# Optimization experiments

Measured on AMD Instinct MI355X. Metric: run time of the kernel, lower is better.

Reference implementation:

```python
import jax, jax.numpy as jnp
import numpy as np

L = 2        # n_layers
IN = 172     # in_channels
HID = 128    # hidden_channels
NH = 4       # heads
HD = HID // NH  # per-head dim = 32
TD = 100     # time_dim
V = 400000   # global node table size
N = 150000   # sampled subgraph nodes
E = 500000   # edges per layer
B = 15000    # seed batch size


def setup_inputs() -> dict:
    key = jax.random.key(0)
    ks = jax.random.split(key, 24)
    p = lambda k, shp, s=0.05: jax.random.normal(k, shp, jnp.float32) * s
    inp = {
        "x_all": jax.random.normal(ks[0], (V, IN), jnp.float32),
        "all_node_ids": jax.random.randint(ks[1], (N,), 0, V),
        "edge_src": jax.random.randint(ks[2], (L, E), 0, N),
        "edge_dst": jax.random.randint(ks[3], (L, E), 0, N),
        "dts": jax.random.uniform(ks[4], (L, E), jnp.float32, 0.0, 1e4),
        "batch_size": B,
        # TimeEncode params
        "basis_freq": jnp.asarray(1.0 / 10 ** np.linspace(0, 9, TD), jnp.float32),
        "phase": jnp.zeros((TD,), jnp.float32),
        # input projection
        "Wp": p(ks[5], (IN, HID)), "bp": jnp.zeros((HID,), jnp.float32),
        # per-layer TransformerConv params (stacked over L)
        "Wq": p(ks[6], (L, HID, HID)), "bq": jnp.zeros((L, HID), jnp.float32),
        "Wk": p(ks[7], (L, HID, HID)), "bk": jnp.zeros((L, HID), jnp.float32),
        "Wv": p(ks[8], (L, HID, HID)), "bv": jnp.zeros((L, HID), jnp.float32),
        "We": p(ks[9], (L, TD, HID)),  # lin_edge, bias=False in PyG
        "Wskip": p(ks[10], (L, HID, HID)), "bskip": jnp.zeros((L, HID), jnp.float32),
        "bn_g": jnp.ones((L, HID), jnp.float32), "bn_b": jnp.zeros((L, HID), jnp.float32),
        # classifier head
        "W1": p(ks[11], (HID, HID)), "b1": jnp.zeros((HID,), jnp.float32),
        "g1": jnp.ones((HID,), jnp.float32), "be1": jnp.zeros((HID,), jnp.float32),
        "W2": p(ks[12], (HID, HID // 2)), "b2": jnp.zeros((HID // 2,), jnp.float32),
        "g2": jnp.ones((HID // 2,), jnp.float32), "be2": jnp.zeros((HID // 2,), jnp.float32),
        "W3": p(ks[13], (HID // 2, 1)), "b3": jnp.zeros((1,), jnp.float32),
    }
    return inp


def _bn(x, g, b):
    # BatchNorm1d, training-mode batch statistics (biased variance), eps=1e-5
    m = x.mean(0)
    v = x.var(0)
    return g * (x - m) * jax.lax.rsqrt(v + 1e-5) + b


def reference(x_all, all_node_ids, edge_src, edge_dst, dts, batch_size,
              basis_freq, phase, Wp, bp, Wq, bq, Wk, bk, Wv, bv, We,
              Wskip, bskip, bn_g, bn_b, W1, b1, g1, be1, W2, b2, g2, be2, W3, b3):
    n = all_node_ids.shape[0]
    x = x_all[all_node_ids]                      # [N, IN] gather from global table
    h = jax.nn.relu(x @ Wp + bp)                 # [N, HID]
    inv_sqrt_d = 1.0 / np.sqrt(HD)
    for i in range(L):
        src, dst, dt = edge_src[i], edge_dst[i], dts[i]
        # learnable sinusoidal time encoding of edge delta-t  [E, TD]
        te = jnp.cos(dt[:, None] * basis_freq[None, :] + phase[None, :])
        q = (h @ Wq[i] + bq[i]).reshape(n, NH, HD)
        k = (h @ Wk[i] + bk[i]).reshape(n, NH, HD)
        v = (h @ Wv[i] + bv[i]).reshape(n, NH, HD)
        e = (te @ We[i]).reshape(-1, NH, HD)     # [E, NH, HD]
        kj = k[src] + e                          # key + edge proj (PyG TransformerConv)
        vj = v[src] + e                          # value + edge proj
        alpha = jnp.einsum('ehd,ehd->eh', q[dst], kj) * inv_sqrt_d  # [E, NH]
        # scatter-softmax over edges grouped by destination node
        m = jax.ops.segment_max(alpha, dst, num_segments=n)
        a = jnp.exp(alpha - m[dst])
        s = jax.ops.segment_sum(a, dst, num_segments=n) + 1e-16
        w = a / s[dst]                           # [E, NH]
        agg = jax.ops.segment_sum(w[:, :, None] * vj, dst, num_segments=n)
        out = agg.reshape(n, HID) + h @ Wskip[i] + bskip[i]  # concat heads + root skip
        h = _bn(jax.nn.relu(out), bn_g[i], bn_b[i])          # dropout = identity (eval)
    hb = h[:batch_size]
    z = jax.nn.relu(_bn(hb @ W1 + b1, g1, be1))
    z = jax.nn.relu(_bn(z @ W2 + b2, g2, be2))
    return (z @ W3 + b3)[:, 0]                   # [batch_size]
```

## Files before the change

kernel.cpp:

```cpp
#include <hip/hip_runtime.h>
#include <hip/hip_bf16.h>
#include <math.h>

#define IN_DIM 172
#define HID 128
#define TDIM 100
#define KPAD 192

typedef __attribute__((ext_vector_type(8))) short bf16x8;
typedef __attribute__((ext_vector_type(4))) float f32x4;

static __device__ __forceinline__ ushort f2b(float x) {
  unsigned u = __float_as_uint(x);
  u += 0x7FFFu + ((u >> 16) & 1u);
  return (ushort)(u >> 16);
}
static __device__ __forceinline__ float blo(unsigned w) { return __uint_as_float(w << 16); }
static __device__ __forceinline__ float bhi(unsigned w) { return __uint_as_float(w & 0xffff0000u); }

__global__ void k_prep(const float* __restrict__ Wp,
                       const float* __restrict__ Wq, const float* __restrict__ Wk,
                       const float* __restrict__ Wv, const float* __restrict__ Ws,
                       const float* __restrict__ bq, const float* __restrict__ bk,
                       const float* __restrict__ bv, const float* __restrict__ bs,
                       const float* __restrict__ We, const float* __restrict__ W1,
                       ushort* __restrict__ wpt,
                       ushort* __restrict__ wallT0, ushort* __restrict__ wallT1,
                       float* __restrict__ ball0, float* __restrict__ ball1,
                       ushort* __restrict__ wet0, ushort* __restrict__ wet1,
                       ushort* __restrict__ w1t) {
  int i = blockIdx.x * 256 + threadIdx.x;
  if (i < 128 * KPAD) {
    int c = i / KPAD, k = i - c * KPAD;
    wpt[i] = (k < IN_DIM) ? f2b(Wp[k * HID + c]) : (ushort)0;
    return;
  }
  i -= 128 * KPAD;
  if (i < 2 * 512 * 128) {
    int layer = i >> 16;
    int j = i & 65535;
    int col = j >> 7, k = j & 127;
    int m = col >> 7, c = col & 127;
    const float* W = (m == 0) ? Wq : (m == 1) ? Wk : (m == 2) ? Wv : Ws;
    W += (size_t)layer * HID * HID;
    (layer ? wallT1 : wallT0)[j] = f2b(W[k * HID + c]);
    if (k == 0) {
      const float* bb = (m == 0) ? bq : (m == 1) ? bk : (m == 2) ? bv : bs;
      (layer ? ball1 : ball0)[col] = bb[layer * HID + c];
    }
    return;
  }
  i -= 2 * 512 * 128;
  if (i < 2 * 128 * 128) {
    int layer = i >> 14;
    int j = i & 16383;
    int c = j >> 7, t = j & 127;
    (layer ? wet1 : wet0)[j] =
        (t < TDIM) ? f2b(We[((size_t)layer * TDIM + t) * HID + c]) : (ushort)0;
    return;
  }
  i -= 2 * 128 * 128;
  if (i < 128 * 128) {
    int c = i >> 7, k = i & 127;
    w1t[i] = f2b(W1[k * HID + c]);
  }
}

__global__ __launch_bounds__(256) void k_in_mfma(
    const float* __restrict__ x_all, const int* __restrict__ ids,
    const ushort* __restrict__ wpt, const float* __restrict__ bp,
    ushort* __restrict__ h, int n) {
  __shared__ __align__(16) ushort xs[64][200];
  int tid = threadIdx.x;
  long r0 = (long)blockIdx.x * 64;
  for (int i = tid; i < 64 * 28; i += 256) {
    int r = i / 28, c = IN_DIM + (i - r * 28);
    xs[r][c] = 0;
  }
  for (int i = tid; i < 64 * 43; i += 256) {
    int r = i / 43, seg = i - r * 43;
    long row = r0 + r;
    float4 v = make_float4(0.f, 0.f, 0.f, 0.f);
    if (row < n) v = *(const float4*)(x_all + (size_t)ids[row] * IN_DIM + seg * 4);
    ushort4 u;
    u.x = f2b(v.x); u.y = f2b(v.y); u.z = f2b(v.z); u.w = f2b(v.w);
    *(ushort4*)&xs[r][seg * 4] = u;
  }
  __syncthreads();
  int wv = tid >> 6, l = tid & 63;
  int arow = wv * 16 + (l & 15);
  int kb0 = (l >> 4) * 8;
  bf16x8 a[6];
  #pragma unroll
  for (int kk = 0; kk < 6; ++kk) a[kk] = *(const bf16x8*)&xs[arow][kk * 32 + kb0];
  #pragma unroll
  for (int nt = 0; nt < 8; ++nt) {
    int col = nt * 16 + (l & 15);
    const ushort* wcol = wpt + (size_t)col * KPAD + kb0;
    f32x4 acc = {0.f, 0.f, 0.f, 0.f};
    #pragma unroll
    for (int kk = 0; kk < 6; ++kk) {
      bf16x8 bfr = *(const bf16x8*)(wcol + kk * 32);
      acc = __builtin_amdgcn_mfma_f32_16x16x32_bf16(a[kk], bfr, acc, 0, 0, 0);
    }
    float bias = bp[col];
    #pragma unroll
    for (int j = 0; j < 4; ++j) {
      long row = r0 + wv * 16 + (l >> 4) * 4 + j;
      if (row < n) {
        float y = acc[j] + bias;
        h[row * HID + col] = f2b(y > 0.f ? y : 0.f);
      }
    }
  }
}

template <bool BN_IN>
__global__ __launch_bounds__(512) void k_qkvs(
    const ushort* __restrict__ hbf, const float* __restrict__ xf,
    const float* __restrict__ sums, const float* __restrict__ bng,
    const float* __restrict__ bnb, float inv_n,
    const ushort* __restrict__ wallT, const float* __restrict__ ball,
    ushort* __restrict__ qb, ushort* __restrict__ kbuf, ushort* __restrict__ vb,
    float* __restrict__ ob, int n) {
  __shared__ __align__(16) ushort hs[128][136];
  __shared__ __align__(16) ushort ws[64][136];
  __shared__ float As[128], Bs[128];
  int tid = threadIdx.x;
  if (BN_IN) {
    if (tid < 128) {
      float mean = sums[tid] * inv_n;
      float var = sums[128 + tid] * inv_n - mean * mean;
      float A = bng[tid] * rsqrtf(var + 1e-5f);
      As[tid] = A;
      Bs[tid] = bnb[tid] - mean * A;
    }
    __syncthreads();
  }
  long r0 = (long)blockIdx.x * 128;
  for (int i = tid; i < 128 * 16; i += 512) {
    int r = i >> 4, cseg = i & 15;
    long row = r0 + r;
    int c0 = cseg * 8;
    if (BN_IN) {
      ushort4 ua = {0, 0, 0, 0}, ub = {0, 0, 0, 0};
      if (row < n) {
        const float* xr = xf + row * HID + c0;
        float4 xa = *(const float4*)xr;
        float4 xb = *(const float4*)(xr + 4);
        ua.x = f2b(As[c0 + 0] * fmaxf(xa.x, 0.f) + Bs[c0 + 0]);
        ua.y = f2b(As[c0 + 1] * fmaxf(xa.y, 0.f) + Bs[c0 + 1]);
        ua.z = f2b(As[c0 + 2] * fmaxf(xa.z, 0.f) + Bs[c0 + 2]);
        ua.w = f2b(As[c0 + 3] * fmaxf(xa.w, 0.f) + Bs[c0 + 3]);
        ub.x = f2b(As[c0 + 4] * fmaxf(xb.x, 0.f) + Bs[c0 + 4]);
        ub.y = f2b(As[c0 + 5] * fmaxf(xb.y, 0.f) + Bs[c0 + 5]);
        ub.z = f2b(As[c0 + 6] * fmaxf(xb.z, 0.f) + Bs[c0 + 6]);
        ub.w = f2b(As[c0 + 7] * fmaxf(xb.w, 0.f) + Bs[c0 + 7]);
      }
      *(ushort4*)&hs[r][c0] = ua;
      *(ushort4*)&hs[r][c0 + 4] = ub;
    } else {
      bf16x8 zv = {0, 0, 0, 0, 0, 0, 0, 0};
      bf16x8 v = (row < n) ? *(const bf16x8*)&hbf[row * HID + c0] : zv;
      *(bf16x8*)&hs[r][c0] = v;
    }
  }
  __syncthreads();
  int wv = tid >> 6, l = tid & 63;
  int arow = wv * 16 + (l & 15);
  int kb0 = (l >> 4) * 8;
  bf16x8 a[4];
  #pragma unroll
  for (int kk = 0; kk < 4; ++kk) a[kk] = *(const bf16x8*)&hs[arow][kk * 32 + kb0];

  for (int g = 0; g < 8; ++g) {
    __syncthreads();
    for (int i = tid; i < 64 * 16; i += 512) {
      int c = i >> 4, cseg = i & 15;
      *(bf16x8*)&ws[c][cseg * 8] =
          *(const bf16x8*)&wallT[(size_t)(g * 64 + c) * 128 + cseg * 8];
    }
    __syncthreads();
    #pragma unroll
    for (int nt = 0; nt < 4; ++nt) {
      int colc = nt * 16 + (l & 15);
      int gcol = g * 64 + colc;
      f32x4 acc = {0.f, 0.f, 0.f, 0.f};
      #pragma unroll
      for (int kk = 0; kk < 4; ++kk) {
        bf16x8 bfr = *(const bf16x8*)&ws[colc][kk * 32 + kb0];
        acc = __builtin_amdgcn_mfma_f32_16x16x32_bf16(a[kk], bfr, acc, 0, 0, 0);
      }
      float bias = ball[gcol];
      int m = gcol >> 7, c = gcol & 127;
      #pragma unroll
      for (int j = 0; j < 4; ++j) {
        long row = r0 + wv * 16 + (l >> 4) * 4 + j;
        if (row < n) {
          float y = acc[j] + bias;
          if (m == 3) ob[row * HID + c] = y;
          else {
            ushort* db = (m == 0) ? qb : (m == 1) ? kbuf : vb;
            db[row * HID + c] = f2b(y);
          }
        }
      }
    }
  }
}

__global__ __launch_bounds__(256) void k_mfma128_bn(
    const float* __restrict__ xf, const float* __restrict__ sums,
    const float* __restrict__ bng, const float* __restrict__ bnb, float inv_n,
    const ushort* __restrict__ WT, const float* __restrict__ bias,
    float* __restrict__ Y, int n) {
  __shared__ __align__(16) ushort hs[64][136];
  __shared__ float As[128], Bs[128];
  int tid = threadIdx.x;
  if (tid < 128) {
    float mean = sums[tid] * inv_n;
    float var = sums[128 + tid] * inv_n - mean * mean;
    float A = bng[tid] * rsqrtf(var + 1e-5f);
    As[tid] = A;
    Bs[tid] = bnb[tid] - mean * A;
  }
  __syncthreads();
  long r0 = (long)blockIdx.x * 64;
  for (int i = tid; i < 64 * 16; i += 256) {
    int r = i >> 4, cseg = i & 15;
    long row = r0 + r;
    int c0 = cseg * 8;
    ushort4 ua = {0, 0, 0, 0}, ub = {0, 0, 0, 0};
    if (row < n) {
      const float* xr = xf + row * HID + c0;
      float4 xa = *(const float4*)xr;
      float4 xb = *(const float4*)(xr + 4);
      ua.x = f2b(As[c0 + 0] * fmaxf(xa.x, 0.f) + Bs[c0 + 0]);
      ua.y = f2b(As[c0 + 1] * fmaxf(xa.y, 0.f) + Bs[c0 + 1]);
      ua.z = f2b(As[c0 + 2] * fmaxf(xa.z, 0.f) + Bs[c0 + 2]);
      ua.w = f2b(As[c0 + 3] * fmaxf(xa.w, 0.f) + Bs[c0 + 3]);
      ub.x = f2b(As[c0 + 4] * fmaxf(xb.x, 0.f) + Bs[c0 + 4]);
      ub.y = f2b(As[c0 + 5] * fmaxf(xb.y, 0.f) + Bs[c0 + 5]);
      ub.z = f2b(As[c0 + 6] * fmaxf(xb.z, 0.f) + Bs[c0 + 6]);
      ub.w = f2b(As[c0 + 7] * fmaxf(xb.w, 0.f) + Bs[c0 + 7]);
    }
    *(ushort4*)&hs[r][c0] = ua;
    *(ushort4*)&hs[r][c0 + 4] = ub;
  }
  __syncthreads();
  int wv = tid >> 6, l = tid & 63;
  int arow = wv * 16 + (l & 15);
  int kb0 = (l >> 4) * 8;
  bf16x8 a[4];
  #pragma unroll
  for (int kk = 0; kk < 4; ++kk) a[kk] = *(const bf16x8*)&hs[arow][kk * 32 + kb0];
  #pragma unroll
  for (int nt = 0; nt < 8; ++nt) {
    int col = nt * 16 + (l & 15);
    const ushort* wcol = WT + (size_t)col * 128 + kb0;
    f32x4 acc = {0.f, 0.f, 0.f, 0.f};
    #pragma unroll
    for (int kk = 0; kk < 4; ++kk) {
      bf16x8 bfr = *(const bf16x8*)(wcol + kk * 32);
      acc = __builtin_amdgcn_mfma_f32_16x16x32_bf16(a[kk], bfr, acc, 0, 0, 0);
    }
    float bs = bias[col];
    #pragma unroll
    for (int j = 0; j < 4; ++j) {
      long row = r0 + wv * 16 + (l >> 4) * 4 + j;
      if (row < n) Y[row * HID + col] = acc[j] + bs;
    }
  }
}

__global__ void k_hist(const int* __restrict__ dst, int* __restrict__ counts, int nE) {
  int e = blockIdx.x * 256 + threadIdx.x;
  if (e < nE) atomicAdd(&counts[dst[e]], 1);
}

__global__ void k_scan_chunk(const int* __restrict__ counts, int* __restrict__ offs,
                             int* __restrict__ chunkSums, int n) {
  __shared__ int ls[256];
  int t = threadIdx.x;
  int base = blockIdx.x * 1024 + t * 4;
  int v[4];
  #pragma unroll
  for (int j = 0; j < 4; ++j) v[j] = (base + j < n) ? counts[base + j] : 0;
  ls[t] = v[0] + v[1] + v[2] + v[3];
  __syncthreads();
  for (int off = 1; off < 256; off <<= 1) {
    int x = (t >= off) ? ls[t - off] : 0;
    __syncthreads();
    ls[t] += x;
    __syncthreads();
  }
  int run = (t == 0) ? 0 : ls[t - 1];
  if (t == 255) chunkSums[blockIdx.x] = ls[255];
  #pragma unroll
  for (int j = 0; j < 4; ++j) {
    if (base + j < n) offs[base + j] = run;
    run += v[j];
  }
}

__global__ void k_scan_tops(int* __restrict__ chunkSums, int nchunks) {
  __shared__ int ls[256];
  int t = threadIdx.x;
  ls[t] = (t < nchunks) ? chunkSums[t] : 0;
  __syncthreads();
  for (int off = 1; off < 256; off <<= 1) {
    int x = (t >= off) ? ls[t - off] : 0;
    __syncthreads();
    ls[t] += x;
    __syncthreads();
  }
  int excl = (t == 0) ? 0 : ls[t - 1];
  if (t < nchunks) chunkSums[t] = excl;
}

__global__ void k_scan_add(int* __restrict__ offs, const int* __restrict__ chunkSums,
                           int n, int nE) {
  int i = blockIdx.x * 256 + threadIdx.x;
  if (i < n) offs[i] += chunkSums[i >> 10];
  if (i == 0) offs[n] = nE;
}

__global__ void k_scatter(const int* __restrict__ src, const int* __restrict__ dst,
                          const float* __restrict__ dts, const int* __restrict__ offs,
                          int* __restrict__ cursor, uint2* __restrict__ edata, int nE) {
  int e = blockIdx.x * 256 + threadIdx.x;
  if (e >= nE) return;
  int d = dst[e];
  int pos = offs[d] + atomicAdd(&cursor[d], 1);
  edata[pos] = make_uint2((unsigned)src[e], __float_as_uint(dts[e]));
}

__global__ __launch_bounds__(256) void k_te_mfma(
    const uint2* __restrict__ edata, const float* __restrict__ freq,
    const float* __restrict__ phase, const ushort* __restrict__ wet,
    ushort* __restrict__ eb, int nE) {
  __shared__ __align__(16) ushort te[64][136];
  __shared__ float dt_s[64];
  __shared__ float fr_s[128], ph_s[128];
  int tid = threadIdx.x;
  if (tid < 128) {
    fr_s[tid] = (tid < TDIM) ? freq[tid] : 0.f;
    ph_s[tid] = (tid < TDIM) ? phase[tid] : 0.f;
  }
  long e0 = (long)blockIdx.x << 6;
  if (tid < 64) dt_s[tid] = (e0 + tid < nE) ? __uint_as_float(edata[e0 + tid].y) : 0.f;
  __syncthreads();
  for (int i = tid; i < 64 * 128; i += 256) {
    int el = i >> 7, t = i & 127;
    float val = (t < TDIM) ? __cosf(dt_s[el] * fr_s[t] + ph_s[t]) : 0.f;
    te[el][t] = f2b(val);
  }
  __syncthreads();
  int wv = tid >> 6, l = tid & 63;
  int arow = wv * 16 + (l & 15);
  int kb0 = (l >> 4) * 8;
  bf16x8 a[4];
  #pragma unroll
  for (int kk = 0; kk < 4; ++kk) a[kk] = *(const bf16x8*)&te[arow][kk * 32 + kb0];
  #pragma unroll
  for (int nt = 0; nt < 8; ++nt) {
    int col = nt * 16 + (l & 15);
    const ushort* wcol = wet + (size_t)col * 128 + kb0;
    f32x4 acc = {0.f, 0.f, 0.f, 0.f};
    #pragma unroll
    for (int kk = 0; kk < 4; ++kk) {
      bf16x8 bfr = *(const bf16x8*)(wcol + kk * 32);
      acc = __builtin_amdgcn_mfma_f32_16x16x32_bf16(a[kk], bfr, acc, 0, 0, 0);
    }
    #pragma unroll
    for (int j = 0; j < 4; ++j) {
      long row = e0 + wv * 16 + (l >> 4) * 4 + j;
      if (row < nE) eb[row * 128 + col] = f2b(acc[j]);
    }
  }
}

__global__ void k_attn(const int* __restrict__ offs, const uint2* __restrict__ edata,
                       const ushort* __restrict__ eb, const ushort* __restrict__ qb,
                       const ushort* __restrict__ kb, const ushort* __restrict__ vb,
                       float* __restrict__ ob, int n) {
  int d = (blockIdx.x * 256 + threadIdx.x) >> 6;
  if (d >= n) return;
  int lane = threadIdx.x & 63;
  int sub = lane >> 4;
  int cl = lane & 15;
  int c0 = cl * 8;
  int beg = offs[d], end = offs[d + 1];
  if (beg == end) return;
  uint4 qw = *(const uint4*)(qb + (size_t)d * HID + c0);
  float q0 = blo(qw.x), q1 = bhi(qw.x), q2 = blo(qw.y), q3 = bhi(qw.y);
  float q4 = blo(qw.z), q5 = bhi(qw.z), q6 = blo(qw.w), q7 = bhi(qw.w);
  float m = -INFINITY, s = 0.f;
  float a0 = 0.f, a1 = 0.f, a2 = 0.f, a3 = 0.f, a4 = 0.f, a5 = 0.f, a6 = 0.f, a7 = 0.f;
  for (int base = beg; base < end; base += 4) {
    int pos = base + sub;
    bool valid = pos < end;
    int pp = valid ? pos : beg;
    int sv = (int)edata[pp].x;
    uint4 kw = *(const uint4*)(kb + (size_t)sv * HID + c0);
    uint4 vw = *(const uint4*)(vb + (size_t)sv * HID + c0);
    uint4 ew = *(const uint4*)(eb + (size_t)pp * HID + c0);
    float e0 = blo(ew.x), e1 = bhi(ew.x), e2 = blo(ew.y), e3 = bhi(ew.y);
    float e4 = blo(ew.z), e5 = bhi(ew.z), e6 = blo(ew.w), e7 = bhi(ew.w);
    float p = q0 * (blo(kw.x) + e0) + q1 * (bhi(kw.x) + e1) +
              q2 * (blo(kw.y) + e2) + q3 * (bhi(kw.y) + e3) +
              q4 * (blo(kw.z) + e4) + q5 * (bhi(kw.z) + e5) +
              q6 * (blo(kw.w) + e6) + q7 * (bhi(kw.w) + e7);
    p += __shfl_xor(p, 1);
    p += __shfl_xor(p, 2);
    float av = valid ? p * 0.17677669529663687f : -INFINITY;
    float nm = fmaxf(m, av);
    float sc = (m > -INFINITY) ? __expf(m - nm) : 0.f;
    float pe = valid ? __expf(av - nm) : 0.f;
    m = nm;
    s = s * sc + pe;
    a0 = a0 * sc + pe * (blo(vw.x) + e0);
    a1 = a1 * sc + pe * (bhi(vw.x) + e1);
    a2 = a2 * sc + pe * (blo(vw.y) + e2);
    a3 = a3 * sc + pe * (bhi(vw.y) + e3);
    a4 = a4 * sc + pe * (blo(vw.z) + e4);
    a5 = a5 * sc + pe * (bhi(vw.z) + e5);
    a6 = a6 * sc + pe * (blo(vw.w) + e6);
    a7 = a7 * sc + pe * (bhi(vw.w) + e7);
  }
  #pragma unroll
  for (int off = 16; off <= 32; off <<= 1) {
    float mo = __shfl_xor(m, off);
    float so = __shfl_xor(s, off);
    float t0 = __shfl_xor(a0, off), t1 = __shfl_xor(a1, off);
    float t2 = __shfl_xor(a2, off), t3 = __shfl_xor(a3, off);
    float t4 = __shfl_xor(a4, off), t5 = __shfl_xor(a5, off);
    float t6 = __shfl_xor(a6, off), t7 = __shfl_xor(a7, off);
    float nm = fmaxf(m, mo);
    float s1 = (m > -INFINITY) ? __expf(m - nm) : 0.f;
    float s2 = (mo > -INFINITY) ? __expf(mo - nm) : 0.f;
    s = s * s1 + so * s2;
    a0 = a0 * s1 + t0 * s2; a1 = a1 * s1 + t1 * s2;
    a2 = a2 * s1 + t2 * s2; a3 = a3 * s1 + t3 * s2;
    a4 = a4 * s1 + t4 * s2; a5 = a5 * s1 + t5 * s2;
    a6 = a6 * s1 + t6 * s2; a7 = a7 * s1 + t7 * s2;
    m = nm;
  }
  if (sub == 0) {
    float inv = 1.f / (s + 1e-16f);
    float4* o = (float4*)(ob + (size_t)d * HID + c0);
    float4 x0 = o[0], x1 = o[1];
    x0.x += a0 * inv; x0.y += a1 * inv; x0.z += a2 * inv; x0.w += a3 * inv;
    x1.x += a4 * inv; x1.y += a5 * inv; x1.z += a6 * inv; x1.w += a7 * inv;
    o[0] = x0; o[1] = x1;
  }
}

template <bool PRE_RELU>
__global__ void k_bn_reduce(const float* __restrict__ X, int n, int C, int shift,
                            float* __restrict__ sums) {
  int col = threadIdx.x & (C - 1);
  int rloc = threadIdx.x >> shift;
  int rpt = 256 >> shift;
  float s = 0.f, s2 = 0.f;
  for (long r = (long)blockIdx.x * rpt + rloc; r < n; r += (long)gridDim.x * rpt) {
    float v = X[r * C + col];
    if (PRE_RELU) v = v > 0.f ? v : 0.f;
    s += v; s2 += v * v;
  }
  __shared__ float ls[256], ls2[256];
  ls[threadIdx.x] = s; ls2[threadIdx.x] = s2;
  __syncthreads();
  if (rloc == 0) {
    for (int j = 1; j < rpt; ++j) { s += ls[j * C + col]; s2 += ls2[j * C + col]; }
    atomicAdd(&sums[col], s);
    atomicAdd(&sums[C + col], s2);
  }
}

__global__ __launch_bounds__(256) void k_gemm_64(
    const float* __restrict__ X, const float* __restrict__ sums,
    const float* __restrict__ g, const float* __restrict__ be, float inv_n,
    const float* __restrict__ W, const float* __restrict__ b,
    float* __restrict__ Y, int n) {
  __shared__ float xs[16][HID];
  __shared__ float As[128], Bs[128];
  if (threadIdx.x < 128) {
    int c = threadIdx.x;
    float mean = sums[c] * inv_n;
    float var = sums[128 + c] * inv_n - mean * mean;
    float A = g[c] * rsqrtf(var + 1e-5f);
    As[c] = A;
    Bs[c] = be[c] - mean * A;
  }
  __syncthreads();
  int r0 = blockIdx.x * 16;
  for (int idx = threadIdx.x; idx < 16 * HID; idx += 256) {
    int r = idx >> 7, c = idx & 127;
    int row = r0 + r;
    float v = (row < n) ? X[(size_t)row * HID + c] : 0.f;
    v = As[c] * v + Bs[c];
    xs[r][c] = v > 0.f ? v : 0.f;
  }
  __syncthreads();
  int col = threadIdx.x & 63;
  int rg = threadIdx.x >> 6;
  float acc[4] = {0.f, 0.f, 0.f, 0.f};
  #pragma unroll 4
  for (int kk = 0; kk < HID; ++kk) {
    float w = W[kk * 64 + col];
    #pragma unroll
    for (int j = 0; j < 4; ++j) acc[j] += xs[rg + 4 * j][kk] * w;
  }
  float bias = b[col];
  #pragma unroll
  for (int j = 0; j < 4; ++j) {
    int row = r0 + rg + 4 * j;
    if (row < n) Y[(size_t)row * 64 + col] = acc[j] + bias;
  }
}

__global__ __launch_bounds__(256) void k_final(
    const float* __restrict__ z2, const float* __restrict__ sums,
    const float* __restrict__ g2, const float* __restrict__ be2, float inv_n,
    const float* __restrict__ W3, const float* __restrict__ b3,
    float* __restrict__ out, int n) {
  int wave = threadIdx.x >> 6, lane = threadIdx.x & 63;
  int row = blockIdx.x * 4 + wave;
  if (row >= n) return;
  float z = z2[(size_t)row * 64 + lane];
  float mean = sums[lane] * inv_n;
  float var = sums[64 + lane] * inv_n - mean * mean;
  float v = g2[lane] * (z - mean) * rsqrtf(var + 1e-5f) + be2[lane];
  v = v > 0.f ? v : 0.f;
  float pv = v * W3[lane];
  pv += __shfl_xor(pv, 1);
  pv += __shfl_xor(pv, 2);
  pv += __shfl_xor(pv, 4);
  pv += __shfl_xor(pv, 8);
  pv += __shfl_xor(pv, 16);
  pv += __shfl_xor(pv, 32);
  if (lane == 0) out[row] = pv + b3[0];
}

extern "C" void kernel_launch(void* const* d_in, const int* in_sizes, int n_in,
                              void* d_out, int out_size, void* d_ws, size_t ws_size,
                              hipStream_t stream) {
  const float* x_all = (const float*)d_in[0];
  const int* ids = (const int*)d_in[1];
  const int* esrc = (const int*)d_in[2];
  const int* edst = (const int*)d_in[3];
  const float* dts = (const float*)d_in[4];
  const float* freq = (const float*)d_in[6];
  const float* phase = (const float*)d_in[7];
  const float* Wp = (const float*)d_in[8];
  const float* bp = (const float*)d_in[9];
  const float* Wq = (const float*)d_in[10];
  const float* bq = (const float*)d_in[11];
  const float* Wk = (const float*)d_in[12];
  const float* bk = (const float*)d_in[13];
  const float* Wv = (const float*)d_in[14];
  const float* bv = (const float*)d_in[15];
  const float* We = (const float*)d_in[16];
  const float* Wskip = (const float*)d_in[17];
  const float* bskip = (const float*)d_in[18];
  const float* bn_g = (const float*)d_in[19];
  const float* bn_b = (const float*)d_in[20];
  const float* W1 = (const float*)d_in[21];
  const float* b1 = (const float*)d_in[22];
  const float* g1 = (const float*)d_in[23];
  const float* be1 = (const float*)d_in[24];
  const float* W2 = (const float*)d_in[25];
  const float* b2 = (const float*)d_in[26];
  const float* g2 = (const float*)d_in[27];
  const float* be2 = (const float*)d_in[28];
  const float* W3 = (const float*)d_in[29];
  const float* b3 = (const float*)d_in[30];

  size_t n = (size_t)in_sizes[1];
  size_t nE = (size_t)in_sizes[2] / 2;
  int B = out_size;

  char* pc = (char*)d_ws;
  auto alloc = [&](size_t bytes) { char* r = pc; pc += (bytes + 255) & ~(size_t)255; return r; };
  ushort* h    = (ushort*)alloc(n * HID * 2);
  ushort* qb   = (ushort*)alloc(n * HID * 2);
  ushort* kb   = (ushort*)alloc(n * HID * 2);
  ushort* vb   = (ushort*)alloc(n * HID * 2);
  float*  ob0  = (float*)alloc(n * HID * 4);
  float*  ob1  = (float*)alloc(n * HID * 4);
  ushort* eb   = (ushort*)alloc(nE * HID * 2);
  uint2* edata = (uint2*)alloc(nE * 8);
  int* offs    = (int*)alloc((n + 1) * 4);
  int* chunkS  = (int*)alloc(256 * 4);
  size_t zbytes = 4 * n * 4 + 4 * 256 * 4;
  char* zb = alloc(zbytes);
  int* counts0 = (int*)zb;
  int* cursor0 = counts0 + n;
  int* counts1 = cursor0 + n;
  int* cursor1 = counts1 + n;
  float* sumsL0 = (float*)(cursor1 + n);
  float* sumsL1 = sumsL0 + 256;
  float* sumsZ1 = sumsL1 + 256;
  float* sumsZ2 = sumsZ1 + 256;
  ushort* wpt    = (ushort*)alloc(128 * KPAD * 2);
  ushort* wallT0 = (ushort*)alloc(512 * 128 * 2);
  ushort* wallT1 = (ushort*)alloc(512 * 128 * 2);
  float* ball0   = (float*)alloc(512 * 4);
  float* ball1   = (float*)alloc(512 * 4);
  ushort* wet0   = (ushort*)alloc(128 * 128 * 2);
  ushort* wet1   = (ushort*)alloc(128 * 128 * 2);
  ushort* w1t    = (ushort*)alloc(128 * 128 * 2);
  float* z1      = (float*)alloc((size_t)B * HID * 4);
  float* z2      = (float*)alloc((size_t)B * 64 * 4);

  int gn64 = (int)((n + 63) / 64);
  int gn128 = (int)((n + 127) / 128);
  int ge256 = (int)((nE + 255) / 256);
  int eblk = (int)((nE + 63) / 64);
  int nchunks = (int)((n + 1023) / 1024);
  float inv_nf = 1.f / (float)n;
  float inv_bf = 1.f / (float)B;

  hipMemsetAsync(zb, 0, zbytes, stream);
  k_prep<<<(128 * KPAD + 2 * 512 * 128 + 2 * 128 * 128 + 128 * 128 + 255) / 256, 256, 0, stream>>>(
      Wp, Wq, Wk, Wv, Wskip, bq, bk, bv, bskip, We, W1,
      wpt, wallT0, wallT1, ball0, ball1, wet0, wet1, w1t);
  k_in_mfma<<<gn64, 256, 0, stream>>>(x_all, ids, wpt, bp, h, (int)n);

  for (int i = 0; i < 2; ++i) {
    const int* src_i = esrc + i * nE;
    const int* dst_i = edst + i * nE;
    const float* dts_i = dts + i * nE;
    int* counts = i ? counts1 : counts0;
    int* cursor = i ? cursor1 : cursor0;
    const ushort* wallT = i ? wallT1 : wallT0;
    const float* ball = i ? ball1 : ball0;
    const ushort* wet = i ? wet1 : wet0;
    float* ob = i ? ob1 : ob0;

    if (i == 0)
      k_qkvs<false><<<gn128, 512, 0, stream>>>(h, nullptr, nullptr, nullptr, nullptr, 0.f,
                                               wallT, ball, qb, kb, vb, ob, (int)n);
    else
      k_qkvs<true><<<gn128, 512, 0, stream>>>(nullptr, ob0, sumsL0, bn_g, bn_b, inv_nf,
                                              wallT, ball, qb, kb, vb, ob, (int)n);

    k_hist<<<ge256, 256, 0, stream>>>(dst_i, counts, (int)nE);
    k_scan_chunk<<<nchunks, 256, 0, stream>>>(counts, offs, chunkS, (int)n);
    k_scan_tops<<<1, 256, 0, stream>>>(chunkS, nchunks);
    k_scan_add<<<(int)((n + 255) / 256), 256, 0, stream>>>(offs, chunkS, (int)n, (int)nE);
    k_scatter<<<ge256, 256, 0, stream>>>(src_i, dst_i, dts_i, offs, cursor, edata, (int)nE);
    k_te_mfma<<<eblk, 256, 0, stream>>>(edata, freq, phase, wet, eb, (int)nE);
    k_attn<<<(int)((n + 3) / 4), 256, 0, stream>>>(offs, edata, eb, qb, kb, vb, ob, (int)n);
    k_bn_reduce<true><<<512, 256, 0, stream>>>(ob, (int)n, HID, 7, i ? sumsL1 : sumsL0);
  }

  k_mfma128_bn<<<(B + 63) / 64, 256, 0, stream>>>(ob1, sumsL1, bn_g + HID, bn_b + HID,
                                                  inv_nf, w1t, b1, z1, B);
  k_bn_reduce<false><<<512, 256, 0, stream>>>(z1, B, HID, 7, sumsZ1);
  k_gemm_64<<<(B + 15) / 16, 256, 0, stream>>>(z1, sumsZ1, g1, be1, inv_bf, W2, b2, z2, B);
  k_bn_reduce<false><<<512, 256, 0, stream>>>(z2, B, 64, 6, sumsZ2);
  k_final<<<(B + 3) / 4, 256, 0, stream>>>(z2, sumsZ2, g2, be2, inv_bf, W3, b3,
                                           (float*)d_out, B);
}
```

Baseline: 1.023 ms.

## Interleave K/V storage, batch CSR build for both layers, register-resident QKVS weights

K and V are stored interleaved in one buffer, so each gathered source row fetches K and V from adjacent memory. The histogram, scan and scatter for both layers are merged into single launches over a combined 2n segment space, which removes the per-layer launch overhead. The QKVS GEMM now keeps each wave's 64 weight columns in registers and loops over row tiles, dropping the per-group LDS weight staging and its barriers. The cost is higher register pressure and larger CSR and edge buffers.

Result: no change. 1.030 ms (+0.7%).

```diff
diff --git a/kernel.cpp b/kernel.cpp
--- a/kernel.cpp
+++ b/kernel.cpp
@@ -121,10 +121,9 @@
     const float* __restrict__ sums, const float* __restrict__ bng,
     const float* __restrict__ bnb, float inv_n,
     const ushort* __restrict__ wallT, const float* __restrict__ ball,
-    ushort* __restrict__ qb, ushort* __restrict__ kbuf, ushort* __restrict__ vb,
+    ushort* __restrict__ qb, ushort* __restrict__ kvb,
     float* __restrict__ ob, int n) {
   __shared__ __align__(16) ushort hs[128][136];
-  __shared__ __align__(16) ushort ws[64][136];
   __shared__ float As[128], Bs[128];
   int tid = threadIdx.x;
   if (BN_IN) {
@@ -165,44 +164,48 @@
       *(bf16x8*)&hs[r][c0] = v;
     }
   }
-  __syncthreads();
   int wv = tid >> 6, l = tid & 63;
-  int arow = wv * 16 + (l & 15);
   int kb0 = (l >> 4) * 8;
-  bf16x8 a[4];
-  #pragma unroll
-  for (int kk = 0; kk < 4; ++kk) a[kk] = *(const bf16x8*)&hs[arow][kk * 32 + kb0];
-
-  for (int g = 0; g < 8; ++g) {
-    __syncthreads();
-    for (int i = tid; i < 64 * 16; i += 512) {
-      int c = i >> 4, cseg = i & 15;
-      *(bf16x8*)&ws[c][cseg * 8] =
-          *(const bf16x8*)&wallT[(size_t)(g * 64 + c) * 128 + cseg * 8];
-    }
-    __syncthreads();
-    #pragma unroll
-    for (int nt = 0; nt < 4; ++nt) {
-      int colc = nt * 16 + (l & 15);
-      int gcol = g * 64 + colc;
-      f32x4 acc = {0.f, 0.f, 0.f, 0.f};
+  int Cw = wv * 64;
+  int m = wv >> 1;
+  bf16x8 b[4][4];
+  float bias4[4];
+  #pragma unroll
+  for (int ct = 0; ct < 4; ++ct) {
+    int col = Cw + ct * 16 + (l & 15);
+    bias4[ct] = ball[col];
+    #pragma unroll
+    for (int kk = 0; kk < 4; ++kk)
+      b[ct][kk] = *(const bf16x8*)&wallT[(size_t)col * 128 + kk * 32 + kb0];
+  }
+  __syncthreads();
+  #pragma unroll 2
+  for (int rt = 0; rt < 8; ++rt) {
+    bf16x8 a[4];
+    #pragma unroll
+    for (int kk = 0; kk < 4; ++kk)
+      a[kk] = *(const bf16x8*)&hs[rt * 16 + (l & 15)][kk * 32 + kb0];
+    f32x4 acc[4];
+    #pragma unroll
+    for (int ct = 0; ct < 4; ++ct) acc[ct] = (f32x4){0.f, 0.f, 0.f, 0.f};
+    #pragma unroll
+    for (int kk = 0; kk < 4; ++kk) {
       #pragma unroll
-      for (int kk = 0; kk < 4; ++kk) {
-        bf16x8 bfr = *(const bf16x8*)&ws[colc][kk * 32 + kb0];
-        acc = __builtin_amdgcn_mfma_f32_16x16x32_bf16(a[kk], bfr, acc, 0, 0, 0);
-      }
-      float bias = ball[gcol];
-      int m = gcol >> 7, c = gcol & 127;
+      for (int ct = 0; ct < 4; ++ct)
+        acc[ct] = __builtin_amdgcn_mfma_f32_16x16x32_bf16(a[kk], b[ct][kk], acc[ct], 0, 0, 0);
+    }
+    #pragma unroll
+    for (int ct = 0; ct < 4; ++ct) {
+      int cc = (wv & 1) * 64 + ct * 16 + (l & 15);
       #pragma unroll
       for (int j = 0; j < 4; ++j) {
-        long row = r0 + wv * 16 + (l >> 4) * 4 + j;
+        long row = r0 + rt * 16 + (l >> 4) * 4 + j;
         if (row < n) {
-          float y = acc[j] + bias;
-          if (m == 3) ob[row * HID + c] = y;
-          else {
-            ushort* db = (m == 0) ? qb : (m == 1) ? kbuf : vb;
-            db[row * HID + c] = f2b(y);
-          }
+          float y = acc[ct][j] + bias4[ct];
+          if (m == 0) qb[row * HID + cc] = f2b(y);
+          else if (m == 1) kvb[row * 256 + cc] = f2b(y);
+          else if (m == 2) kvb[row * 256 + 128 + cc] = f2b(y);
+          else ob[row * HID + cc] = y;
         }
       }
     }
@@ -273,19 +276,22 @@
   }
 }
 
-__global__ void k_hist(const int* __restrict__ dst, int* __restrict__ counts, int nE) {
+__global__ void k_hist2(const int* __restrict__ dst_all, int* __restrict__ counts,
+                        int n, int nE2, int nE) {
   int e = blockIdx.x * 256 + threadIdx.x;
-  if (e < nE) atomicAdd(&counts[dst[e]], 1);
+  if (e >= nE2) return;
+  int layer = (e >= nE) ? 1 : 0;
+  atomicAdd(&counts[layer * n + dst_all[e]], 1);
 }
 
 __global__ void k_scan_chunk(const int* __restrict__ counts, int* __restrict__ offs,
-                             int* __restrict__ chunkSums, int n) {
+                             int* __restrict__ chunkSums, int m) {
   __shared__ int ls[256];
   int t = threadIdx.x;
   int base = blockIdx.x * 1024 + t * 4;
   int v[4];
   #pragma unroll
-  for (int j = 0; j < 4; ++j) v[j] = (base + j < n) ? counts[base + j] : 0;
+  for (int j = 0; j < 4; ++j) v[j] = (base + j < m) ? counts[base + j] : 0;
   ls[t] = v[0] + v[1] + v[2] + v[3];
   __syncthreads();
   for (int off = 1; off < 256; off <<= 1) {
@@ -298,17 +304,17 @@
   if (t == 255) chunkSums[blockIdx.x] = ls[255];
   #pragma unroll
   for (int j = 0; j < 4; ++j) {
-    if (base + j < n) offs[base + j] = run;
+    if (base + j < m) offs[base + j] = run;
     run += v[j];
   }
 }
 
-__global__ void k_scan_tops(int* __restrict__ chunkSums, int nchunks) {
-  __shared__ int ls[256];
+__global__ __launch_bounds__(512) void k_scan_tops(int* __restrict__ chunkSums, int nchunks) {
+  __shared__ int ls[512];
   int t = threadIdx.x;
   ls[t] = (t < nchunks) ? chunkSums[t] : 0;
   __syncthreads();
-  for (int off = 1; off < 256; off <<= 1) {
+  for (int off = 1; off < 512; off <<= 1) {
     int x = (t >= off) ? ls[t - off] : 0;
     __syncthreads();
     ls[t] += x;
@@ -319,20 +325,22 @@
 }
 
 __global__ void k_scan_add(int* __restrict__ offs, const int* __restrict__ chunkSums,
-                           int n, int nE) {
+                           int m, int totalE) {
   int i = blockIdx.x * 256 + threadIdx.x;
-  if (i < n) offs[i] += chunkSums[i >> 10];
-  if (i == 0) offs[n] = nE;
-}
-
-__global__ void k_scatter(const int* __restrict__ src, const int* __restrict__ dst,
-                          const float* __restrict__ dts, const int* __restrict__ offs,
-                          int* __restrict__ cursor, uint2* __restrict__ edata, int nE) {
+  if (i < m) offs[i] += chunkSums[i >> 10];
+  if (i == 0) offs[m] = totalE;
+}
+
+__global__ void k_scatter2(const int* __restrict__ src_all, const int* __restrict__ dst_all,
+                           const float* __restrict__ dts_all, const int* __restrict__ offs,
+                           int* __restrict__ cursor, uint2* __restrict__ edata,
+                           int n, int nE2, int nE) {
   int e = blockIdx.x * 256 + threadIdx.x;
-  if (e >= nE) return;
-  int d = dst[e];
+  if (e >= nE2) return;
+  int layer = (e >= nE) ? 1 : 0;
+  int d = layer * n + dst_all[e];
   int pos = offs[d] + atomicAdd(&cursor[d], 1);
-  edata[pos] = make_uint2((unsigned)src[e], __float_as_uint(dts[e]));
+  edata[pos] = make_uint2((unsigned)src_all[e], __float_as_uint(dts_all[e]));
 }
 
 __global__ __launch_bounds__(256) void k_te_mfma(
@@ -380,9 +388,9 @@
   }
 }
 
-__global__ void k_attn(const int* __restrict__ offs, const uint2* __restrict__ edata,
-                       const ushort* __restrict__ eb, const ushort* __restrict__ qb,
-                       const ushort* __restrict__ kb, const ushort* __restrict__ vb,
+__global__ void k_attn(const int* __restrict__ offs_l, const uint2* __restrict__ edata,
+                       int bias, const ushort* __restrict__ eb,
+                       const ushort* __restrict__ qb, const ushort* __restrict__ kvb,
                        float* __restrict__ ob, int n) {
   int d = (blockIdx.x * 256 + threadIdx.x) >> 6;
   if (d >= n) return;
@@ -390,8 +398,9 @@
   int sub = lane >> 4;
   int cl = lane & 15;
   int c0 = cl * 8;
-  int beg = offs[d], end = offs[d + 1];
+  int beg = offs_l[d], end = offs_l[d + 1];
   if (beg == end) return;
+  const ushort* ebl = eb - (size_t)bias * HID;
   uint4 qw = *(const uint4*)(qb + (size_t)d * HID + c0);
   float q0 = blo(qw.x), q1 = bhi(qw.x), q2 = blo(qw.y), q3 = bhi(qw.y);
   float q4 = blo(qw.z), q5 = bhi(qw.z), q6 = blo(qw.w), q7 = bhi(qw.w);
@@ -402,9 +411,9 @@
     bool valid = pos < end;
     int pp = valid ? pos : beg;
     int sv = (int)edata[pp].x;
-    uint4 kw = *(const uint4*)(kb + (size_t)sv * HID + c0);
-    uint4 vw = *(const uint4*)(vb + (size_t)sv * HID + c0);
-    uint4 ew = *(const uint4*)(eb + (size_t)pp * HID + c0);
+    uint4 kw = *(const uint4*)(kvb + (size_t)sv * 256 + c0);
+    uint4 vw = *(const uint4*)(kvb + (size_t)sv * 256 + 128 + c0);
+    uint4 ew = *(const uint4*)(ebl + (size_t)pp * HID + c0);
     float e0 = blo(ew.x), e1 = bhi(ew.x), e2 = blo(ew.y), e3 = bhi(ew.y);
     float e4 = blo(ew.z), e5 = bhi(ew.z), e6 = blo(ew.w), e7 = bhi(ew.w);
     float p = q0 * (blo(kw.x) + e0) + q1 * (bhi(kw.x) + e1) +
@@ -579,27 +588,25 @@
 
   size_t n = (size_t)in_sizes[1];
   size_t nE = (size_t)in_sizes[2] / 2;
+  size_t nE2 = nE * 2;
   int B = out_size;
 
   char* pc = (char*)d_ws;
   auto alloc = [&](size_t bytes) { char* r = pc; pc += (bytes + 255) & ~(size_t)255; return r; };
   ushort* h    = (ushort*)alloc(n * HID * 2);
   ushort* qb   = (ushort*)alloc(n * HID * 2);
-  ushort* kb   = (ushort*)alloc(n * HID * 2);
-  ushort* vb   = (ushort*)alloc(n * HID * 2);
+  ushort* kvb  = (ushort*)alloc(n * 256 * 2);
   float*  ob0  = (float*)alloc(n * HID * 4);
   float*  ob1  = (float*)alloc(n * HID * 4);
   ushort* eb   = (ushort*)alloc(nE * HID * 2);
-  uint2* edata = (uint2*)alloc(nE * 8);
-  int* offs    = (int*)alloc((n + 1) * 4);
-  int* chunkS  = (int*)alloc(256 * 4);
+  uint2* edata = (uint2*)alloc(nE2 * 8);
+  int* offs    = (int*)alloc((2 * n + 2) * 4);
+  int* chunkS  = (int*)alloc(512 * 4);
   size_t zbytes = 4 * n * 4 + 4 * 256 * 4;
   char* zb = alloc(zbytes);
-  int* counts0 = (int*)zb;
-  int* cursor0 = counts0 + n;
-  int* counts1 = cursor0 + n;
-  int* cursor1 = counts1 + n;
-  float* sumsL0 = (float*)(cursor1 + n);
+  int* counts = (int*)zb;
+  int* cursor = counts + 2 * n;
+  float* sumsL0 = (float*)(cursor + 2 * n);
   float* sumsL1 = sumsL0 + 256;
   float* sumsZ1 = sumsL1 + 256;
   float* sumsZ2 = sumsZ1 + 256;
@@ -616,9 +623,10 @@
 
   int gn64 = (int)((n + 63) / 64);
   int gn128 = (int)((n + 127) / 128);
-  int ge256 = (int)((nE + 255) / 256);
+  int ge2 = (int)((nE2 + 255) / 256);
   int eblk = (int)((nE + 63) / 64);
-  int nchunks = (int)((n + 1023) / 1024);
+  int m2 = (int)(2 * n);
+  int nchunks = (m2 + 1023) / 1024;
   float inv_nf = 1.f / (float)n;
   float inv_bf = 1.f / (float)B;
 
@@ -628,31 +636,30 @@
       wpt, wallT0, wallT1, ball0, ball1, wet0, wet1, w1t);
   k_in_mfma<<<gn64, 256, 0, stream>>>(x_all, ids, wpt, bp, h, (int)n);
 
+  k_hist2<<<ge2, 256, 0, stream>>>(edst, counts, (int)n, (int)nE2, (int)nE);
+  k_scan_chunk<<<nchunks, 256, 0, stream>>>(counts, offs, chunkS, m2);
+  k_scan_tops<<<1, 512, 0, stream>>>(chunkS, nchunks);
+  k_scan_add<<<(m2 + 255) / 256, 256, 0, stream>>>(offs, chunkS, m2, (int)nE2);
+  k_scatter2<<<ge2, 256, 0, stream>>>(esrc, edst, dts, offs, cursor, edata,
+                                      (int)n, (int)nE2, (int)nE);
+
   for (int i = 0; i < 2; ++i) {
-    const int* src_i = esrc + i * nE;
-    const int* dst_i = edst + i * nE;
-    const float* dts_i = dts + i * nE;
-    int* counts = i ? counts1 : counts0;
-    int* cursor = i ? cursor1 : cursor0;
     const ushort* wallT = i ? wallT1 : wallT0;
     const float* ball = i ? ball1 : ball0;
     const ushort* wet = i ? wet1 : wet0;
     float* ob = i ? ob1 : ob0;
+    int bias = i * (int)nE;
 
     if (i == 0)
       k_qkvs<false><<<gn128, 512, 0, stream>>>(h, nullptr, nullptr, nullptr, nullptr, 0.f,
-                                               wallT, ball, qb, kb, vb, ob, (int)n);
+                                               wallT, ball, qb, kvb, ob, (int)n);
     else
       k_qkvs<true><<<gn128, 512, 0, stream>>>(nullptr, ob0, sumsL0, bn_g, bn_b, inv_nf,
-                                              wallT, ball, qb, kb, vb, ob, (int)n);
-
-    k_hist<<<ge256, 256, 0, stream>>>(dst_i, counts, (int)nE);
-    k_scan_chunk<<<nchunks, 256, 0, stream>>>(counts, offs, chunkS, (int)n);
-    k_scan_tops<<<1, 256, 0, stream>>>(chunkS, nchunks);
-    k_scan_add<<<(int)((n + 255) / 256), 256, 0, stream>>>(offs, chunkS, (int)n, (int)nE);
-    k_scatter<<<ge256, 256, 0, stream>>>(src_i, dst_i, dts_i, offs, cursor, edata, (int)nE);
-    k_te_mfma<<<eblk, 256, 0, stream>>>(edata, freq, phase, wet, eb, (int)nE);
-    k_attn<<<(int)((n + 3) / 4), 256, 0, stream>>>(offs, edata, eb, qb, kb, vb, ob, (int)n);
+                                              wallT, ball, qb, kvb, ob, (int)n);
+
+    k_te_mfma<<<eblk, 256, 0, stream>>>(edata + bias, freq, phase, wet, eb, (int)nE);
+    k_attn<<<(int)((n + 3) / 4), 256, 0, stream>>>(offs + (size_t)i * n, edata, bias,
+                                                   eb, qb, kvb, ob, (int)n);
     k_bn_reduce<true><<<512, 256, 0, stream>>>(ob, (int)n, HID, 7, i ? sumsL1 : sumsL0);
   }
 
```
